# Kernel tuning notes

Hardware: AMD Instinct MI355X
Metric: run time of the kernel (lower is better)

Reference implementation:

```python
import jax, jax.numpy as jnp
import numpy as np


def setup_inputs() -> dict:
    key = jax.random.key(0)
    k1, k2 = jax.random.split(key)
    B, N, M, C = 32, 4096, 4096, 3
    xyz1 = jax.random.normal(k1, (B, N, C), dtype=jnp.float32)
    xyz2 = jax.random.normal(k2, (B, M, C), dtype=jnp.float32)
    return {"xyz1": xyz1, "xyz2": xyz2}


def _chamfer_l2(xyz1, xyz2):
    # Pairwise squared L2 distances via ||a||^2 + ||b||^2 - 2 a.b  (b n m)
    sq1 = jnp.sum(xyz1 * xyz1, axis=-1)            # [B, N]
    sq2 = jnp.sum(xyz2 * xyz2, axis=-1)            # [B, M]
    cross = jnp.einsum('bnc,bmc->bnm', xyz1, xyz2) # [B, N, M]
    d = sq1[:, :, None] + sq2[:, None, :] - 2.0 * cross
    dist1 = jnp.min(d, axis=2)                     # [B, N] nearest in xyz2
    dist2 = jnp.min(d, axis=1)                     # [B, M] nearest in xyz1
    return jnp.mean(dist1, axis=-1) + jnp.mean(dist2, axis=-1)  # [B]


def reference(xyz1, xyz2):
    return _chamfer_l2(xyz1, xyz2)
```

## Files before the change

### kernel.cpp

```cpp
#include <hip/hip_runtime.h>

typedef _Float16 half8 __attribute__((ext_vector_type(8)));
typedef float floatx16 __attribute__((ext_vector_type(16)));

#define TPB    256
#define CHUNK  1024
#define NTILE  (CHUNK / 32)
#define SMH    (CHUNK * 16)


#define FMIN __builtin_fminf

__device__ __forceinline__ float fold16(floatx16 d) {
    float m0 = FMIN(FMIN(d[0],  d[1]),  d[2]);
    float m1 = FMIN(FMIN(d[3],  d[4]),  d[5]);
    float m2 = FMIN(FMIN(d[6],  d[7]),  d[8]);
    float m3 = FMIN(FMIN(d[9],  d[10]), d[11]);
    float m4 = FMIN(FMIN(d[12], d[13]), d[14]);
    float n0 = FMIN(FMIN(m0, m1), m2);
    float n1 = FMIN(FMIN(m3, m4), d[15]);
    return FMIN(n0, n1);
}

__device__ __forceinline__ void wr_point(_Float16* __restrict__ smb, int j,
                                         float x, float y, float z) {
    float hq = 0.5f * (x * x + y * y + z * z);
    _Float16 xh = (_Float16)x, yh = (_Float16)y, zh = (_Float16)z;
    _Float16 xl = (_Float16)(x - (float)xh);
    _Float16 yl = (_Float16)(y - (float)yh);
    _Float16 zl = (_Float16)(z - (float)zh);
    _Float16 qh = (_Float16)hq;
    _Float16 ql = (_Float16)(hq - (float)qh);
    const _Float16 hz = (_Float16)0.0f;
    int t = j >> 5, c = j & 31;
    half8 v0, v1;
    v0[0] = xh; v0[1] = xl; v0[2] = xh; v0[3] = yh;
    v0[4] = yl; v0[5] = yh; v0[6] = zh; v0[7] = zl;
    v1[0] = zh; v1[1] = qh; v1[2] = ql; v1[3] = hz;
    v1[4] = hz; v1[5] = hz; v1[6] = hz; v1[7] = hz;
    *(half8*)&smb[t * 512 + c * 8]       = v0;
    *(half8*)&smb[t * 512 + 256 + c * 8] = v1;
}

__global__ __launch_bounds__(TPB, 4) void chamfer_mfma(const float* __restrict__ xyz1,
                                                       const float* __restrict__ xyz2,
                                                       float* __restrict__ ws,
                                                       int N, int M, int QCAP,
                                                       int nchunks) {
    const int b = blockIdx.y, dir = blockIdx.z;
    const int B = gridDim.y;
    const int qblock = (int)blockIdx.x / nchunks;
    const int chunk  = (int)blockIdx.x % nchunks;
    const float* __restrict__ P = dir ? xyz2 + (size_t)b * M * 3 : xyz1 + (size_t)b * N * 3;
    const float* __restrict__ Q = dir ? xyz1 + (size_t)b * N * 3 : xyz2 + (size_t)b * M * 3;
    const int nq = dir ? M : N;
    const int md = dir ? N : M;

    if (qblock * 256 >= nq) return;

    const int base = chunk * CHUNK;

    __shared__ __align__(16) _Float16 smB[SMH];

    const int tid = (int)threadIdx.x;
    const int w   = tid >> 6;
    const int l   = tid & 63;
    const int m   = l & 31;
    const int h   = l >> 5;

    const _Float16 hz = (_Float16)0.0f, hone = (_Float16)1.0f;
    const int qb = qblock * 256 + w * 64;

    half8 qfr[2];
#pragma unroll
    for (int g = 0; g < 2; ++g) {
        int idx = qb + g * 32 + m;
        int ci  = idx < nq ? idx : nq - 1;
        float x = P[3 * ci], y = P[3 * ci + 1], z = P[3 * ci + 2];
        _Float16 xh = (_Float16)x, yh = (_Float16)y, zh = (_Float16)z;
        _Float16 xl = (_Float16)(x - (float)xh);
        _Float16 yl = (_Float16)(y - (float)yh);
        _Float16 zl = (_Float16)(z - (float)zh);
        half8 a;
        if (h == 0) {
            a[0] = -xh; a[1] = -xh; a[2] = -xl; a[3] = -yh;
            a[4] = -yh; a[5] = -yl; a[6] = -zh; a[7] = -zh;
        } else {
            a[0] = -zl; a[1] = hone; a[2] = hone; a[3] = hz;
            a[4] = hz;  a[5] = hz;   a[6] = hz;  a[7] = hz;
        }
        qfr[g] = a;
    }

    {
        int g0 = base + tid;
        int g1 = base + tid + 256;
        int g2 = base + tid + 512;
        int g3 = base + tid + 768;
        g0 = g0 < md ? g0 : md - 1;
        g1 = g1 < md ? g1 : md - 1;
        g2 = g2 < md ? g2 : md - 1;
        g3 = g3 < md ? g3 : md - 1;
        float x0 = Q[3 * g0], y0 = Q[3 * g0 + 1], z0 = Q[3 * g0 + 2];
        float x1 = Q[3 * g1], y1 = Q[3 * g1 + 1], z1 = Q[3 * g1 + 2];
        float x2 = Q[3 * g2], y2 = Q[3 * g2 + 1], z2 = Q[3 * g2 + 2];
        float x3 = Q[3 * g3], y3 = Q[3 * g3 + 1], z3 = Q[3 * g3 + 2];
        wr_point(smB, tid,       x0, y0, z0);
        wr_point(smB, tid + 256, x1, y1, z1);
        wr_point(smB, tid + 512, x2, y2, z2);
        wr_point(smB, tid + 768, x3, y3, z3);
    }
    __syncthreads();

    float rmq0 = 3.0e38f, rmq1 = 3.0e38f;

    const floatx16 czero = {0.0f, 0.0f, 0.0f, 0.0f, 0.0f, 0.0f, 0.0f, 0.0f,
                            0.0f, 0.0f, 0.0f, 0.0f, 0.0f, 0.0f, 0.0f, 0.0f};

    const _Float16* bp = &smB[h * 256 + m * 8];
    half8 cur = *(const half8*)(bp);
    half8 nx1 = *(const half8*)(bp + 512);
    half8 nx2 = *(const half8*)(bp + 1024);
    floatx16 dp0 = __builtin_amdgcn_mfma_f32_32x32x16_f16(cur, qfr[0], czero, 0, 0, 0);
    floatx16 dp1 = __builtin_amdgcn_mfma_f32_32x32x16_f16(cur, qfr[1], czero, 0, 0, 0);
#pragma unroll 2
    for (int t = 1; t <= NTILE; ++t) {
        cur = nx1;
        nx1 = nx2;
        nx2 = *(const half8*)(bp + ((t + 2) & (NTILE - 1)) * 512);
        floatx16 dc0 = __builtin_amdgcn_mfma_f32_32x32x16_f16(cur, qfr[0], czero, 0, 0, 0);
        floatx16 dc1 = __builtin_amdgcn_mfma_f32_32x32x16_f16(cur, qfr[1], czero, 0, 0, 0);
        rmq0 = FMIN(rmq0, fold16(dp0));
        rmq1 = FMIN(rmq1, fold16(dp1));
        dp0 = dc0; dp1 = dc1;
    }
    rmq0 = FMIN(rmq0, fold16(dp0));
    rmq1 = FMIN(rmq1, fold16(dp1));

    rmq0 = FMIN(rmq0, __shfl_xor(rmq0, 32, 64));
    rmq1 = FMIN(rmq1, __shfl_xor(rmq1, 32, 64));

    float* __restrict__ wsd = ws + (((size_t)chunk * 2 + dir) * B + b) * QCAP;
    const int idx = qb + l;
    const float val = h ? rmq1 : rmq0;
    if (idx < nq) wsd[idx] = val;
}

__global__ __launch_bounds__(256) void chamfer_reduce(const float* __restrict__ xyz1,
                                                      const float* __restrict__ xyz2,
                                                      const float* __restrict__ ws,
                                                      float* __restrict__ out,
                                                      int N, int M, int QCAP,
                                                      int nchunks) {
    const int b = (int)blockIdx.x, dir = (int)blockIdx.y;
    const int B = gridDim.x;
    const float* __restrict__ P = dir ? xyz2 + (size_t)b * M * 3 : xyz1 + (size_t)b * N * 3;
    const int nq = dir ? M : N;
    const size_t cs = (size_t)2 * B * QCAP;
    const float* __restrict__ w0 = ws + ((size_t)dir * B + b) * QCAP;

    float s = 0.0f;
    for (int q = (int)threadIdx.x + (int)blockIdx.z * 256; q < nq; q += 256 * (int)gridDim.z) {
        float v = w0[q];
        for (int c = 1; c < nchunks; ++c) v = FMIN(v, w0[c * cs + q]);
        float x = P[3 * q], y = P[3 * q + 1], z = P[3 * q + 2];
        s += v + 0.5f * (x * x + y * y + z * z);
    }
#pragma unroll
    for (int off = 32; off > 0; off >>= 1) s += __shfl_down(s, off, 64);
    __shared__ float red[4];
    if ((threadIdx.x & 63) == 0) red[threadIdx.x >> 6] = s;
    __syncthreads();
    if (threadIdx.x == 0) {
        float t = (red[0] + red[1]) + (red[2] + red[3]);
        atomicAdd(out + b, t * (2.0f / (float)nq));
    }
}

extern "C" void kernel_launch(void* const* d_in, const int* in_sizes, int n_in,
                              void* d_out, int out_size, void* d_ws, size_t ws_size,
                              hipStream_t stream) {
    const float* xyz1 = (const float*)d_in[0];
    const float* xyz2 = (const float*)d_in[1];
    float* out = (float*)d_out;

    const int B = out_size;
    const int N = in_sizes[0] / (3 * B);
    const int M = in_sizes[1] / (3 * B);

    hipMemsetAsync(d_out, 0, (size_t)B * sizeof(float), stream);

    const int qmax    = N > M ? N : M;
    const int qblocks = (qmax + 255) / 256;
    const int QCAP    = qblocks * 256;
    const int nchunks = (qmax + CHUNK - 1) / CHUNK;

    dim3 grid(qblocks * nchunks, B, 2);
    chamfer_mfma<<<grid, dim3(TPB), 0, stream>>>(xyz1, xyz2, (float*)d_ws, N, M, QCAP, nchunks);
    chamfer_reduce<<<dim3(B, 2, 4), dim3(256), 0, stream>>>(xyz1, xyz2, (float*)d_ws, out, N, M, QCAP, nchunks);
}
```

Before: 100.2 us.

## Process 512 queries per block with four MFMA fragments per wave

Doubles the queries handled per block so each wave computes four query fragments against every shared B tile, reusing each LDS load and the shared-memory staging of the point chunk across twice as many MFMAs. Halves the grid, and replaces the two-deep software pipeline with a simpler single-prefetch loop interleaving four MFMAs with min-folds. Increases accumulator register pressure and removes explicit unroll, which could reduce latency hiding.

```diff
diff --git a/kernel.cpp b/kernel.cpp
--- a/kernel.cpp
+++ b/kernel.cpp
@@ -4,6 +4,7 @@
 typedef float floatx16 __attribute__((ext_vector_type(16)));
 
 #define TPB    256
+#define QPB    512
 #define CHUNK  1024
 #define NTILE  (CHUNK / 32)
 #define SMH    (CHUNK * 16)
@@ -56,7 +57,7 @@
     const int nq = dir ? M : N;
     const int md = dir ? N : M;
 
-    if (qblock * 256 >= nq) return;
+    if (qblock * QPB >= nq) return;
 
     const int base = chunk * CHUNK;
 
@@ -69,11 +70,11 @@
     const int h   = l >> 5;
 
     const _Float16 hz = (_Float16)0.0f, hone = (_Float16)1.0f;
-    const int qb = qblock * 256 + w * 64;
-
-    half8 qfr[2];
+    const int qb = qblock * QPB + w * 128;
+
+    half8 qfr[4];
 #pragma unroll
-    for (int g = 0; g < 2; ++g) {
+    for (int g = 0; g < 4; ++g) {
         int idx = qb + g * 32 + m;
         int ci  = idx < nq ? idx : nq - 1;
         float x = P[3 * ci], y = P[3 * ci + 1], z = P[3 * ci + 2];
@@ -113,37 +114,39 @@
     __syncthreads();
 
     float rmq0 = 3.0e38f, rmq1 = 3.0e38f;
+    float rmq2 = 3.0e38f, rmq3 = 3.0e38f;
 
     const floatx16 czero = {0.0f, 0.0f, 0.0f, 0.0f, 0.0f, 0.0f, 0.0f, 0.0f,
                             0.0f, 0.0f, 0.0f, 0.0f, 0.0f, 0.0f, 0.0f, 0.0f};
 
     const _Float16* bp = &smB[h * 256 + m * 8];
     half8 cur = *(const half8*)(bp);
-    half8 nx1 = *(const half8*)(bp + 512);
-    half8 nx2 = *(const half8*)(bp + 1024);
-    floatx16 dp0 = __builtin_amdgcn_mfma_f32_32x32x16_f16(cur, qfr[0], czero, 0, 0, 0);
-    floatx16 dp1 = __builtin_amdgcn_mfma_f32_32x32x16_f16(cur, qfr[1], czero, 0, 0, 0);
-#pragma unroll 2
-    for (int t = 1; t <= NTILE; ++t) {
-        cur = nx1;
-        nx1 = nx2;
-        nx2 = *(const half8*)(bp + ((t + 2) & (NTILE - 1)) * 512);
-        floatx16 dc0 = __builtin_amdgcn_mfma_f32_32x32x16_f16(cur, qfr[0], czero, 0, 0, 0);
-        floatx16 dc1 = __builtin_amdgcn_mfma_f32_32x32x16_f16(cur, qfr[1], czero, 0, 0, 0);
-        rmq0 = FMIN(rmq0, fold16(dp0));
-        rmq1 = FMIN(rmq1, fold16(dp1));
-        dp0 = dc0; dp1 = dc1;
-    }
-    rmq0 = FMIN(rmq0, fold16(dp0));
-    rmq1 = FMIN(rmq1, fold16(dp1));
+#pragma unroll 1
+    for (int t = 0; t < NTILE; ++t) {
+        half8 nx = *(const half8*)(bp + ((t + 1) & (NTILE - 1)) * 512);
+        floatx16 d0 = __builtin_amdgcn_mfma_f32_32x32x16_f16(cur, qfr[0], czero, 0, 0, 0);
+        floatx16 d1 = __builtin_amdgcn_mfma_f32_32x32x16_f16(cur, qfr[1], czero, 0, 0, 0);
+        rmq0 = FMIN(rmq0, fold16(d0));
+        floatx16 d2 = __builtin_amdgcn_mfma_f32_32x32x16_f16(cur, qfr[2], czero, 0, 0, 0);
+        rmq1 = FMIN(rmq1, fold16(d1));
+        floatx16 d3 = __builtin_amdgcn_mfma_f32_32x32x16_f16(cur, qfr[3], czero, 0, 0, 0);
+        rmq2 = FMIN(rmq2, fold16(d2));
+        rmq3 = FMIN(rmq3, fold16(d3));
+        cur = nx;
+    }
 
     rmq0 = FMIN(rmq0, __shfl_xor(rmq0, 32, 64));
     rmq1 = FMIN(rmq1, __shfl_xor(rmq1, 32, 64));
+    rmq2 = FMIN(rmq2, __shfl_xor(rmq2, 32, 64));
+    rmq3 = FMIN(rmq3, __shfl_xor(rmq3, 32, 64));
 
     float* __restrict__ wsd = ws + (((size_t)chunk * 2 + dir) * B + b) * QCAP;
-    const int idx = qb + l;
-    const float val = h ? rmq1 : rmq0;
-    if (idx < nq) wsd[idx] = val;
+    const int ia = qb + h * 64 + m;
+    const int ib = ia + 32;
+    const float va = h ? rmq2 : rmq0;
+    const float vb = h ? rmq3 : rmq1;
+    if (ia < nq) wsd[ia] = va;
+    if (ib < nq) wsd[ib] = vb;
 }
 
 __global__ __launch_bounds__(256) void chamfer_reduce(const float* __restrict__ xyz1,
@@ -191,8 +194,8 @@
     hipMemsetAsync(d_out, 0, (size_t)B * sizeof(float), stream);
 
     const int qmax    = N > M ? N : M;
-    const int qblocks = (qmax + 255) / 256;
-    const int QCAP    = qblocks * 256;
+    const int qblocks = (qmax + QPB - 1) / QPB;
+    const int QCAP    = ((qmax + 255) / 256) * 256;
     const int nchunks = (qmax + CHUNK - 1) / CHUNK;
 
     dim3 grid(qblocks * nchunks, B, 2);
```

New measurement: 96.75 us (median of 2 runs). -3.5%, faster.
